# Kernel tuning notes

Measured on AMD Instinct MI355X. Metric: run time of the kernel, lower is better.

Reference implementation:

```python
import jax, jax.numpy as jnp
import numpy as np


def _lstm(x_seq, Wih, Whh, bih, bhh, hidden):
    """Single-layer batch_first LSTM, PyTorch gate order (i,f,g,o).
    x_seq: [B, T, D_in]. Returns (outputs [B, T, H], h_T [B, H])."""
    B = x_seq.shape[0]
    h0 = jnp.zeros((B, hidden), x_seq.dtype)
    c0 = jnp.zeros((B, hidden), x_seq.dtype)

    def step(carry, x_t):
        h, c = carry
        gates = x_t @ Wih.T + bih + h @ Whh.T + bhh  # [B, 4H]
        i, f, g, o = jnp.split(gates, 4, axis=-1)
        i = jax.nn.sigmoid(i)
        f = jax.nn.sigmoid(f)
        g = jnp.tanh(g)
        o = jax.nn.sigmoid(o)
        c = f * c + i * g
        h = o * jnp.tanh(c)
        return (h, c), h

    (hT, _), hs = jax.lax.scan(step, (h0, c0), jnp.swapaxes(x_seq, 0, 1))
    return jnp.swapaxes(hs, 0, 1), hT


def setup_inputs() -> dict:
    key = jax.random.key(0)
    ks = jax.random.split(key, 20)
    B, T = 4096, 140
    W = 0.1  # weight scale to keep gates out of saturation
    inp = {"x": jax.random.normal(ks[0], (B, 1, T), jnp.float32)}
    shapes = {
        "Wih_e1": (512, 1), "Whh_e1": (512, 128), "bih_e1": (512,), "bhh_e1": (512,),
        "Wih_e2": (256, 128), "Whh_e2": (256, 64), "bih_e2": (256,), "bhh_e2": (256,),
        "Wih_d1": (512, 64), "Whh_d1": (512, 128), "bih_d1": (512,), "bhh_d1": (512,),
        "Wih_d2": (4, 128), "Whh_d2": (4, 1), "bih_d2": (4,), "bhh_d2": (4,),
    }
    for i, (name, shp) in enumerate(shapes.items()):
        inp[name] = jax.random.normal(ks[i + 1], shp, jnp.float32) * W
    return inp


def reference(x, Wih_e1, Whh_e1, bih_e1, bhh_e1,
              Wih_e2, Whh_e2, bih_e2, bhh_e2,
              Wih_d1, Whh_d1, bih_d1, bhh_d1,
              Wih_d2, Whh_d2, bih_d2, bhh_d2):
    T = 140
    # x: [B,1,140] -> [B,140,1]
    x_enc = x[:, 0, :, None]
    _, h1 = _lstm(x_enc, Wih_e1, Whh_e1, bih_e1, bhh_e1, 128)  # h1: [B,128]
    # faithful to original bug: hn1 [1,B,128] fed as batch_first input (batch=1, seq=B)
    hn1_seq = h1[None, :, :]
    _, z = _lstm(hn1_seq, Wih_e2, Whh_e2, bih_e2, bhh_e2, 64)  # z: [1,64]
    dec_in = jnp.broadcast_to(z[:, None, :], (1, T, 64))
    out1, _ = _lstm(dec_in, Wih_d1, Whh_d1, bih_d1, bhh_d1, 128)  # [1,140,128]
    out2, _ = _lstm(out1, Wih_d2, Whh_d2, bih_d2, bhh_d2, 1)      # [1,140,1]
    recon = out2[..., 0][:, None, :]  # [1,1,140]
    return recon
```

## Files before the change

kernel.cpp:

```cpp
#include <hip/hip_runtime.h>
#include <hip/hip_bf16.h>


__device__ __forceinline__ float sigm(float x) {
  return 1.0f / (1.0f + __expf(-x));
}
__device__ __forceinline__ float tanh_fast(float x) {
  return 1.0f - 2.0f / (__expf(2.0f * x) + 1.0f);
}

__device__ __forceinline__ void wg_barrier() {
  asm volatile("s_waitcnt lgkmcnt(0)\n\ts_barrier" ::: "memory");
}

template <int CTRL>
__device__ __forceinline__ float dppmv(float v) {
  return __int_as_float(__builtin_amdgcn_update_dpp(
      0, __float_as_int(v), CTRL, 0xF, 0xF, true));
}
#define DPP_XOR1   0xB1
#define DPP_XOR2   0x4E
#define DPP_ROT1   0x93
#define DPP_HMIRR  0x141
#define DPP_MIRR   0x140

__device__ __forceinline__ int swzc(int k) { return k + ((k >> 5) << 2); }

#define A_BB 16

__global__ __launch_bounds__(512, 2) void lstm_e1_kernel(
    const float* __restrict__ x,
    const float* __restrict__ Wih,
    const float* __restrict__ Whh,
    const float* __restrict__ bih,
    const float* __restrict__ bhh,
    float* __restrict__ h1_out)
{
  const int j    = threadIdx.x;
  const int lane = j & 63;
  const int w    = j >> 6;
  const int u    = w * 16 + (lane >> 2);
  const int q    = lane & 3;
  const int b0   = blockIdx.x * A_BB;

  __shared__ float Hs[2][A_BB][144];
  __shared__ float xs[2][A_BB];

  for (int i = j; i < A_BB * 144; i += 512) ((float*)Hs[0])[i] = 0.0f;
  if (j < A_BB) xs[0][j] = x[(b0 + j) * 140];

  float wr[4][32];
#pragma unroll
  for (int g = 0; g < 4; ++g)
#pragma unroll
    for (int k = 0; k < 32; k += 4)
      *(float4*)&wr[g][k] = *(const float4*)&Whh[(g * 128 + u) * 128 + q * 32 + k];

  float wih[4], bs[4];
#pragma unroll
  for (int g = 0; g < 4; ++g) {
    wih[g] = Wih[g * 128 + u];
    bs[g]  = bih[g * 128 + u] + bhh[g * 128 + u];
  }

  float c[4]  = {0.f, 0.f, 0.f, 0.f};
  float hr[4] = {0.f, 0.f, 0.f, 0.f};
  __syncthreads();

  int cur = 0;
  for (int t = 0; t < 140; ++t) {
    const int nxt = cur ^ 1;

    float R[4][4];
#pragma unroll
    for (int g = 0; g < 4; ++g)
#pragma unroll
      for (int i = 0; i < 4; ++i) R[g][i] = 0.0f;

#pragma unroll
    for (int s = 0; s < 4; ++s) {
      if (s) {
#pragma unroll
        for (int g = 0; g < 4; ++g)
#pragma unroll
          for (int i = 0; i < 4; ++i) R[g][i] = dppmv<DPP_ROT1>(R[g][i]);
      }
      const int cch = (q - 1 - s) & 3;
      const float* hbase = &Hs[cur][cch * 4][q * 36];
#pragma unroll
      for (int i = 0; i < 4; ++i) {
        const float* hrow = hbase + i * 144;
#pragma unroll
        for (int kk = 0; kk < 8; ++kk) {
          const float4 hv = *(const float4*)&hrow[kk * 4];
#pragma unroll
          for (int g = 0; g < 4; ++g) {
            R[g][i] = __builtin_fmaf(wr[g][kk * 4 + 0], hv.x, R[g][i]);
            R[g][i] = __builtin_fmaf(wr[g][kk * 4 + 1], hv.y, R[g][i]);
            R[g][i] = __builtin_fmaf(wr[g][kk * 4 + 2], hv.z, R[g][i]);
            R[g][i] = __builtin_fmaf(wr[g][kk * 4 + 3], hv.w, R[g][i]);
          }
        }
      }
    }

    if (j < A_BB && (t + 1) < 140) xs[nxt][j] = x[(b0 + j) * 140 + t + 1];

    const float4 xv = *(const float4*)&xs[cur][q * 4];
    const float xa[4] = {xv.x, xv.y, xv.z, xv.w};
#pragma unroll
    for (int i = 0; i < 4; ++i) {
      const float gi = sigm(R[0][i] + __builtin_fmaf(wih[0], xa[i], bs[0]));
      const float gf = sigm(R[1][i] + __builtin_fmaf(wih[1], xa[i], bs[1]));
      const float gg = tanh_fast(R[2][i] + __builtin_fmaf(wih[2], xa[i], bs[2]));
      const float go = sigm(R[3][i] + __builtin_fmaf(wih[3], xa[i], bs[3]));
      c[i]  = gf * c[i] + gi * gg;
      hr[i] = go * tanh_fast(c[i]);
      Hs[nxt][q * 4 + i][swzc(u)] = hr[i];
    }
    wg_barrier();
    cur = nxt;
  }

#pragma unroll
  for (int i = 0; i < 4; ++i)
    h1_out[(b0 + q * 4 + i) * 128 + u] = hr[i];
}

__global__ __launch_bounds__(256, 1) void u_pre_kernel(
    const float* __restrict__ h1,
    const float* __restrict__ Wih,
    const float* __restrict__ bih,
    const float* __restrict__ bhh,
    float* __restrict__ Up)
{
  const int t = blockIdx.x;
  const int j = threadIdx.x;
  __shared__ float hs[128];
  if (j < 128) hs[j] = h1[t * 128 + j];
  __syncthreads();
  float acc = bih[j] + bhh[j];
#pragma unroll
  for (int k = 0; k < 128; k += 4) {
    const float4 hv = *(const float4*)&hs[k];
    const float4 wv = *(const float4*)&Wih[j * 128 + k];
    acc += wv.x * hv.x + wv.y * hv.y + wv.z * hv.z + wv.w * hv.w;
  }
  Up[t * 256 + (j & 63) * 4 + (j >> 6)] = acc;
}

__global__ __launch_bounds__(512, 1) void lstm_e2_scan_kernel(
    const float4* __restrict__ Up,
    const float* __restrict__ Whh,
    float* __restrict__ z_out)
{
  const int j = threadIdx.x;
  const int u = j >> 3;
  const int o = j & 7;

  __shared__ float hb[2][64];

  float wr[4][8];
#pragma unroll
  for (int g = 0; g < 4; ++g) {
    *(float4*)&wr[g][0] = *(const float4*)&Whh[(g * 64 + u) * 64 + o * 8];
    *(float4*)&wr[g][4] = *(const float4*)&Whh[(g * 64 + u) * 64 + o * 8 + 4];
  }

  if (j < 64) hb[0][j] = 0.0f;
  float c = 0.0f, h = 0.0f;

  float4 U0 = Up[u];
  float4 U1 = Up[64 + u];
  __syncthreads();

  int cur = 0;
#pragma unroll 1
  for (int t = 0; t < 4096; t += 2) {
#pragma unroll
    for (int half = 0; half < 2; ++half) {
      const int tp = (t + 2 + half < 4096) ? (t + 2 + half) : 4095;
      const float4 Unew = Up[tp * 64 + u];
      const float4 Ucur = half ? U1 : U0;

      const float4 hv0 = *(const float4*)&hb[cur][o * 8];
      const float4 hv1 = *(const float4*)&hb[cur][o * 8 + 4];
      float a0, a1, a2, a3;
      a0 = wr[0][0] * hv0.x; a1 = wr[1][0] * hv0.x; a2 = wr[2][0] * hv0.x; a3 = wr[3][0] * hv0.x;
      a0 = __builtin_fmaf(wr[0][1], hv0.y, a0); a1 = __builtin_fmaf(wr[1][1], hv0.y, a1);
      a2 = __builtin_fmaf(wr[2][1], hv0.y, a2); a3 = __builtin_fmaf(wr[3][1], hv0.y, a3);
      a0 = __builtin_fmaf(wr[0][2], hv0.z, a0); a1 = __builtin_fmaf(wr[1][2], hv0.z, a1);
      a2 = __builtin_fmaf(wr[2][2], hv0.z, a2); a3 = __builtin_fmaf(wr[3][2], hv0.z, a3);
      a0 = __builtin_fmaf(wr[0][3], hv0.w, a0); a1 = __builtin_fmaf(wr[1][3], hv0.w, a1);
      a2 = __builtin_fmaf(wr[2][3], hv0.w, a2); a3 = __builtin_fmaf(wr[3][3], hv0.w, a3);
      a0 = __builtin_fmaf(wr[0][4], hv1.x, a0); a1 = __builtin_fmaf(wr[1][4], hv1.x, a1);
      a2 = __builtin_fmaf(wr[2][4], hv1.x, a2); a3 = __builtin_fmaf(wr[3][4], hv1.x, a3);
      a0 = __builtin_fmaf(wr[0][5], hv1.y, a0); a1 = __builtin_fmaf(wr[1][5], hv1.y, a1);
      a2 = __builtin_fmaf(wr[2][5], hv1.y, a2); a3 = __builtin_fmaf(wr[3][5], hv1.y, a3);
      a0 = __builtin_fmaf(wr[0][6], hv1.z, a0); a1 = __builtin_fmaf(wr[1][6], hv1.z, a1);
      a2 = __builtin_fmaf(wr[2][6], hv1.z, a2); a3 = __builtin_fmaf(wr[3][6], hv1.z, a3);
      a0 = __builtin_fmaf(wr[0][7], hv1.w, a0); a1 = __builtin_fmaf(wr[1][7], hv1.w, a1);
      a2 = __builtin_fmaf(wr[2][7], hv1.w, a2); a3 = __builtin_fmaf(wr[3][7], hv1.w, a3);

      a0 += dppmv<DPP_XOR1>(a0);  a1 += dppmv<DPP_XOR1>(a1);
      a2 += dppmv<DPP_XOR1>(a2);  a3 += dppmv<DPP_XOR1>(a3);
      a0 += dppmv<DPP_XOR2>(a0);  a1 += dppmv<DPP_XOR2>(a1);
      a2 += dppmv<DPP_XOR2>(a2);  a3 += dppmv<DPP_XOR2>(a3);
      a0 += dppmv<DPP_HMIRR>(a0); a1 += dppmv<DPP_HMIRR>(a1);
      a2 += dppmv<DPP_HMIRR>(a2); a3 += dppmv<DPP_HMIRR>(a3);

      const float gi = sigm(a0 + Ucur.x);
      const float gf = sigm(a1 + Ucur.y);
      const float gg = tanh_fast(a2 + Ucur.z);
      const float go = sigm(a3 + Ucur.w);
      c = gf * c + gi * gg;
      h = go * tanh_fast(c);
      if (o == 0) hb[cur ^ 1][u] = h;
      if (half) U1 = Unew; else U0 = Unew;
      wg_barrier();
      cur ^= 1;
    }
  }
  if (o == 0) z_out[u] = h;
}

__global__ __launch_bounds__(512, 1) void lstm_dec_kernel(
    const float* __restrict__ z,
    const float* __restrict__ Wih1,
    const float* __restrict__ Whh1,
    const float* __restrict__ bih1,
    const float* __restrict__ bhh1,
    const float* __restrict__ Wih2,
    const float* __restrict__ Whh2,
    const float* __restrict__ bih2,
    const float* __restrict__ bhh2,
    float* __restrict__ out)
{
  const int j = threadIdx.x;
  const int u = j >> 2;
  const int q = j & 3;

  __shared__ float hb[2][144];
  __shared__ float zs[64];
  __shared__ float act4[4];

  if (j < 64) zs[j] = z[j];
  if (j < 144) hb[0][j] = 0.0f;
  __syncthreads();

  float wr[4][32];
#pragma unroll
  for (int g = 0; g < 4; ++g)
#pragma unroll
    for (int k = 0; k < 32; k += 4)
      *(float4*)&wr[g][k] = *(const float4*)&Whh1[(g * 128 + u) * 128 + q * 32 + k];

  float pre0[4];
#pragma unroll
  for (int g = 0; g < 4; ++g) {
    float acc = bih1[g * 128 + u] + bhh1[g * 128 + u];
#pragma unroll
    for (int k = 0; k < 64; k += 4) {
      const float4 zv = *(const float4*)&zs[k];
      const float4 wv = *(const float4*)&Wih1[(g * 128 + u) * 64 + k];
      acc += wv.x * zv.x + wv.y * zv.y + wv.z * zv.z + wv.w * zv.w;
    }
    pre0[g] = acc;
  }

  const int g2  = j >> 4;
  const int i16 = j & 15;
  float w2d[8] = {0,0,0,0,0,0,0,0};
  if (j < 64) {
#pragma unroll
    for (int e = 0; e < 8; ++e) w2d[e] = Wih2[g2 * 128 + i16 * 8 + e];
  }
  const float bb2_0 = bih2[0] + bhh2[0], wh2_0 = Whh2[0];
  const float bb2_1 = bih2[1] + bhh2[1], wh2_1 = Whh2[1];
  const float bb2_2 = bih2[2] + bhh2[2], wh2_2 = Whh2[2];
  const float bb2_3 = bih2[3] + bhh2[3], wh2_3 = Whh2[3];

  float c1 = 0.0f;
  float c2 = 0.0f, h2 = 0.0f;

  int cur = 0;
  for (int t = 0; t < 140; ++t) {
    float a0 = 0.f, a1 = 0.f, a2 = 0.f, a3 = 0.f;
#pragma unroll
    for (int kk = 0; kk < 8; ++kk) {
      const float4 hv = *(const float4*)&hb[cur][q * 36 + kk * 4];
      a0 = __builtin_fmaf(wr[0][kk*4+0], hv.x, a0); a0 = __builtin_fmaf(wr[0][kk*4+1], hv.y, a0);
      a0 = __builtin_fmaf(wr[0][kk*4+2], hv.z, a0); a0 = __builtin_fmaf(wr[0][kk*4+3], hv.w, a0);
      a1 = __builtin_fmaf(wr[1][kk*4+0], hv.x, a1); a1 = __builtin_fmaf(wr[1][kk*4+1], hv.y, a1);
      a1 = __builtin_fmaf(wr[1][kk*4+2], hv.z, a1); a1 = __builtin_fmaf(wr[1][kk*4+3], hv.w, a1);
      a2 = __builtin_fmaf(wr[2][kk*4+0], hv.x, a2); a2 = __builtin_fmaf(wr[2][kk*4+1], hv.y, a2);
      a2 = __builtin_fmaf(wr[2][kk*4+2], hv.z, a2); a2 = __builtin_fmaf(wr[2][kk*4+3], hv.w, a2);
      a3 = __builtin_fmaf(wr[3][kk*4+0], hv.x, a3); a3 = __builtin_fmaf(wr[3][kk*4+1], hv.y, a3);
      a3 = __builtin_fmaf(wr[3][kk*4+2], hv.z, a3); a3 = __builtin_fmaf(wr[3][kk*4+3], hv.w, a3);
    }
    a0 += dppmv<DPP_XOR1>(a0); a0 += dppmv<DPP_XOR2>(a0);
    a1 += dppmv<DPP_XOR1>(a1); a1 += dppmv<DPP_XOR2>(a1);
    a2 += dppmv<DPP_XOR1>(a2); a2 += dppmv<DPP_XOR2>(a2);
    a3 += dppmv<DPP_XOR1>(a3); a3 += dppmv<DPP_XOR2>(a3);

    const float gi = sigm(a0 + pre0[0]);
    const float gf = sigm(a1 + pre0[1]);
    const float gg = tanh_fast(a2 + pre0[2]);
    const float go = sigm(a3 + pre0[3]);
    c1 = gf * c1 + gi * gg;
    const float h1v = go * tanh_fast(c1);
    if (q == 0) hb[cur ^ 1][swzc(u)] = h1v;
    wg_barrier();
    cur ^= 1;

    if (j < 64) {
      const int kb = i16 * 8;
      const float4 hA = *(const float4*)&hb[cur][swzc(kb)];
      const float4 hB = *(const float4*)&hb[cur][swzc(kb) + 4];
      float p = hA.x * w2d[0];
      p = __builtin_fmaf(hA.y, w2d[1], p);
      p = __builtin_fmaf(hA.z, w2d[2], p);
      p = __builtin_fmaf(hA.w, w2d[3], p);
      p = __builtin_fmaf(hB.x, w2d[4], p);
      p = __builtin_fmaf(hB.y, w2d[5], p);
      p = __builtin_fmaf(hB.z, w2d[6], p);
      p = __builtin_fmaf(hB.w, w2d[7], p);
      p += dppmv<DPP_XOR1>(p);
      p += dppmv<DPP_XOR2>(p);
      p += dppmv<DPP_HMIRR>(p);
      p += dppmv<DPP_MIRR>(p);
      if (i16 == 0) act4[g2] = p;
      const float4 acts = *(const float4*)&act4[0];
      const float gi2 = sigm(acts.x + bb2_0 + wh2_0 * h2);
      const float gf2 = sigm(acts.y + bb2_1 + wh2_1 * h2);
      const float gg2 = tanh_fast(acts.z + bb2_2 + wh2_2 * h2);
      const float go2 = sigm(acts.w + bb2_3 + wh2_3 * h2);
      c2 = gf2 * c2 + gi2 * gg2;
      h2 = go2 * tanh_fast(c2);
      if (j == 0) out[t] = h2;
    }
  }
}

extern "C" void kernel_launch(void* const* d_in, const int* in_sizes, int n_in,
                              void* d_out, int out_size, void* d_ws, size_t ws_size,
                              hipStream_t stream) {
  const float* x      = (const float*)d_in[0];
  const float* Wih_e1 = (const float*)d_in[1];
  const float* Whh_e1 = (const float*)d_in[2];
  const float* bih_e1 = (const float*)d_in[3];
  const float* bhh_e1 = (const float*)d_in[4];
  const float* Wih_e2 = (const float*)d_in[5];
  const float* Whh_e2 = (const float*)d_in[6];
  const float* bih_e2 = (const float*)d_in[7];
  const float* bhh_e2 = (const float*)d_in[8];
  const float* Wih_d1 = (const float*)d_in[9];
  const float* Whh_d1 = (const float*)d_in[10];
  const float* bih_d1 = (const float*)d_in[11];
  const float* bhh_d1 = (const float*)d_in[12];
  const float* Wih_d2 = (const float*)d_in[13];
  const float* Whh_d2 = (const float*)d_in[14];
  const float* bih_d2 = (const float*)d_in[15];
  const float* bhh_d2 = (const float*)d_in[16];

  float* out = (float*)d_out;

  float* h1 = (float*)d_ws;
  float* Up = h1 + 4096 * 128;
  float* zb = Up + 4096 * 256;

  lstm_e1_kernel<<<4096 / A_BB, 512, 0, stream>>>(x, Wih_e1, Whh_e1, bih_e1, bhh_e1, h1);
  u_pre_kernel<<<4096, 256, 0, stream>>>(h1, Wih_e2, bih_e2, bhh_e2, Up);
  lstm_e2_scan_kernel<<<1, 512, 0, stream>>>((const float4*)Up, Whh_e2, zb);
  lstm_dec_kernel<<<1, 512, 0, stream>>>(zb, Wih_d1, Whh_d1, bih_d1, bhh_d1,
                                         Wih_d2, Whh_d2, bih_d2, bhh_d2, out);
}
```

Baseline: 3.986 ms.

## Use packed FP32 FMA and single-wavefront e2 scan; double units per e1 thread

The encoder-2 scan moves from eight wavefronts with DPP reductions and workgroup barriers to one 64-thread wavefront. Each lane now computes a full 64-wide dot product with packed v_pk_fma_f32 and syncs only through an LDS wait, which targets barrier and reduction latency on the 4096-step serial chain. The e1 kernel halves its thread count, gives each thread two hidden units using packed FMAs, and issues the next x load earlier. The cost is much higher register pressure: e1 now holds 256 weight floats per thread, risking spills or low occupancy. Each e2 step is also a longer dependent FMA chain per lane.

```diff
diff --git a/kernel.cpp b/kernel.cpp
--- a/kernel.cpp
+++ b/kernel.cpp
@@ -2,6 +2,14 @@
 #include <hip/hip_bf16.h>
 
 
+typedef float v2f __attribute__((ext_vector_type(2)));
+
+__device__ __forceinline__ v2f pk_fma(v2f a, v2f b, v2f c) {
+  v2f d;
+  asm("v_pk_fma_f32 %0, %1, %2, %3" : "=v"(d) : "v"(a), "v"(b), "v"(c));
+  return d;
+}
+
 __device__ __forceinline__ float sigm(float x) {
   return 1.0f / (1.0f + __expf(-x));
 }
@@ -11,6 +19,9 @@
 
 __device__ __forceinline__ void wg_barrier() {
   asm volatile("s_waitcnt lgkmcnt(0)\n\ts_barrier" ::: "memory");
+}
+__device__ __forceinline__ void lds_fence() {
+  asm volatile("s_waitcnt lgkmcnt(0)" ::: "memory");
 }
 
 template <int CTRL>
@@ -28,7 +39,7 @@
 
 #define A_BB 16
 
-__global__ __launch_bounds__(512, 2) void lstm_e1_kernel(
+__global__ __launch_bounds__(256, 1) void lstm_e1_kernel(
     const float* __restrict__ x,
     const float* __restrict__ Wih,
     const float* __restrict__ Whh,
@@ -39,43 +50,60 @@
   const int j    = threadIdx.x;
   const int lane = j & 63;
   const int w    = j >> 6;
-  const int u    = w * 16 + (lane >> 2);
+  const int u16  = w * 16 + (lane >> 2);
   const int q    = lane & 3;
+  const int uA   = u16;
+  const int uB   = u16 + 64;
   const int b0   = blockIdx.x * A_BB;
 
   __shared__ float Hs[2][A_BB][144];
   __shared__ float xs[2][A_BB];
 
-  for (int i = j; i < A_BB * 144; i += 512) ((float*)Hs[0])[i] = 0.0f;
+  for (int i = j; i < A_BB * 144; i += 256) ((float*)Hs[0])[i] = 0.0f;
   if (j < A_BB) xs[0][j] = x[(b0 + j) * 140];
 
-  float wr[4][32];
+  v2f wA[4][16], wB[4][16];
 #pragma unroll
   for (int g = 0; g < 4; ++g)
 #pragma unroll
-    for (int k = 0; k < 32; k += 4)
-      *(float4*)&wr[g][k] = *(const float4*)&Whh[(g * 128 + u) * 128 + q * 32 + k];
-
-  float wih[4], bs[4];
+    for (int k = 0; k < 32; k += 4) {
+      const float4 a = *(const float4*)&Whh[(g * 128 + uA) * 128 + q * 32 + k];
+      wA[g][k / 2 + 0].x = a.x; wA[g][k / 2 + 0].y = a.y;
+      wA[g][k / 2 + 1].x = a.z; wA[g][k / 2 + 1].y = a.w;
+      const float4 b = *(const float4*)&Whh[(g * 128 + uB) * 128 + q * 32 + k];
+      wB[g][k / 2 + 0].x = b.x; wB[g][k / 2 + 0].y = b.y;
+      wB[g][k / 2 + 1].x = b.z; wB[g][k / 2 + 1].y = b.w;
+    }
+
+  float wihA[4], bsA[4], wihB[4], bsB[4];
 #pragma unroll
   for (int g = 0; g < 4; ++g) {
-    wih[g] = Wih[g * 128 + u];
-    bs[g]  = bih[g * 128 + u] + bhh[g * 128 + u];
-  }
-
-  float c[4]  = {0.f, 0.f, 0.f, 0.f};
-  float hr[4] = {0.f, 0.f, 0.f, 0.f};
+    wihA[g] = Wih[g * 128 + uA];
+    bsA[g]  = bih[g * 128 + uA] + bhh[g * 128 + uA];
+    wihB[g] = Wih[g * 128 + uB];
+    bsB[g]  = bih[g * 128 + uB] + bhh[g * 128 + uB];
+  }
+
+  float cA[4] = {0,0,0,0}, hA[4] = {0,0,0,0};
+  float cB[4] = {0,0,0,0}, hB[4] = {0,0,0,0};
   __syncthreads();
 
   int cur = 0;
   for (int t = 0; t < 140; ++t) {
     const int nxt = cur ^ 1;
 
-    float R[4][4];
+    float xnext = 0.0f;
+    const bool do_x = (j < A_BB) && (t + 1) < 140;
+    if (do_x) xnext = x[(b0 + j) * 140 + t + 1];
+
+    v2f RA[4][4], RB[4][4];
 #pragma unroll
     for (int g = 0; g < 4; ++g)
 #pragma unroll
-      for (int i = 0; i < 4; ++i) R[g][i] = 0.0f;
+      for (int i = 0; i < 4; ++i) {
+        RA[g][i].x = 0.f; RA[g][i].y = 0.f;
+        RB[g][i].x = 0.f; RB[g][i].y = 0.f;
+      }
 
 #pragma unroll
     for (int s = 0; s < 4; ++s) {
@@ -83,7 +111,12 @@
 #pragma unroll
         for (int g = 0; g < 4; ++g)
 #pragma unroll
-          for (int i = 0; i < 4; ++i) R[g][i] = dppmv<DPP_ROT1>(R[g][i]);
+          for (int i = 0; i < 4; ++i) {
+            RA[g][i].x = dppmv<DPP_ROT1>(RA[g][i].x);
+            RA[g][i].y = dppmv<DPP_ROT1>(RA[g][i].y);
+            RB[g][i].x = dppmv<DPP_ROT1>(RB[g][i].x);
+            RB[g][i].y = dppmv<DPP_ROT1>(RB[g][i].y);
+          }
       }
       const int cch = (q - 1 - s) & 3;
       const float* hbase = &Hs[cur][cch * 4][q * 36];
@@ -93,38 +126,53 @@
 #pragma unroll
         for (int kk = 0; kk < 8; ++kk) {
           const float4 hv = *(const float4*)&hrow[kk * 4];
+          v2f h01; h01.x = hv.x; h01.y = hv.y;
+          v2f h23; h23.x = hv.z; h23.y = hv.w;
 #pragma unroll
           for (int g = 0; g < 4; ++g) {
-            R[g][i] = __builtin_fmaf(wr[g][kk * 4 + 0], hv.x, R[g][i]);
-            R[g][i] = __builtin_fmaf(wr[g][kk * 4 + 1], hv.y, R[g][i]);
-            R[g][i] = __builtin_fmaf(wr[g][kk * 4 + 2], hv.z, R[g][i]);
-            R[g][i] = __builtin_fmaf(wr[g][kk * 4 + 3], hv.w, R[g][i]);
+            RA[g][i] = pk_fma(wA[g][2 * kk + 0], h01, RA[g][i]);
+            RA[g][i] = pk_fma(wA[g][2 * kk + 1], h23, RA[g][i]);
+            RB[g][i] = pk_fma(wB[g][2 * kk + 0], h01, RB[g][i]);
+            RB[g][i] = pk_fma(wB[g][2 * kk + 1], h23, RB[g][i]);
           }
         }
       }
     }
 
-    if (j < A_BB && (t + 1) < 140) xs[nxt][j] = x[(b0 + j) * 140 + t + 1];
+    if (do_x) xs[nxt][j] = xnext;
 
     const float4 xv = *(const float4*)&xs[cur][q * 4];
     const float xa[4] = {xv.x, xv.y, xv.z, xv.w};
 #pragma unroll
     for (int i = 0; i < 4; ++i) {
-      const float gi = sigm(R[0][i] + __builtin_fmaf(wih[0], xa[i], bs[0]));
-      const float gf = sigm(R[1][i] + __builtin_fmaf(wih[1], xa[i], bs[1]));
-      const float gg = tanh_fast(R[2][i] + __builtin_fmaf(wih[2], xa[i], bs[2]));
-      const float go = sigm(R[3][i] + __builtin_fmaf(wih[3], xa[i], bs[3]));
-      c[i]  = gf * c[i] + gi * gg;
-      hr[i] = go * tanh_fast(c[i]);
-      Hs[nxt][q * 4 + i][swzc(u)] = hr[i];
+      {
+        const float gi = sigm(RA[0][i].x + RA[0][i].y + __builtin_fmaf(wihA[0], xa[i], bsA[0]));
+        const float gf = sigm(RA[1][i].x + RA[1][i].y + __builtin_fmaf(wihA[1], xa[i], bsA[1]));
+        const float gg = tanh_fast(RA[2][i].x + RA[2][i].y + __builtin_fmaf(wihA[2], xa[i], bsA[2]));
+        const float go = sigm(RA[3][i].x + RA[3][i].y + __builtin_fmaf(wihA[3], xa[i], bsA[3]));
+        cA[i] = gf * cA[i] + gi * gg;
+        hA[i] = go * tanh_fast(cA[i]);
+        Hs[nxt][q * 4 + i][swzc(uA)] = hA[i];
+      }
+      {
+        const float gi = sigm(RB[0][i].x + RB[0][i].y + __builtin_fmaf(wihB[0], xa[i], bsB[0]));
+        const float gf = sigm(RB[1][i].x + RB[1][i].y + __builtin_fmaf(wihB[1], xa[i], bsB[1]));
+        const float gg = tanh_fast(RB[2][i].x + RB[2][i].y + __builtin_fmaf(wihB[2], xa[i], bsB[2]));
+        const float go = sigm(RB[3][i].x + RB[3][i].y + __builtin_fmaf(wihB[3], xa[i], bsB[3]));
+        cB[i] = gf * cB[i] + gi * gg;
+        hB[i] = go * tanh_fast(cB[i]);
+        Hs[nxt][q * 4 + i][swzc(uB)] = hB[i];
+      }
     }
     wg_barrier();
     cur = nxt;
   }
 
 #pragma unroll
-  for (int i = 0; i < 4; ++i)
-    h1_out[(b0 + q * 4 + i) * 128 + u] = hr[i];
+  for (int i = 0; i < 4; ++i) {
+    h1_out[(b0 + q * 4 + i) * 128 + uA] = hA[i];
+    h1_out[(b0 + q * 4 + i) * 128 + uB] = hB[i];
+  }
 }
 
 __global__ __launch_bounds__(256, 1) void u_pre_kernel(
@@ -149,79 +197,81 @@
   Up[t * 256 + (j & 63) * 4 + (j >> 6)] = acc;
 }
 
-__global__ __launch_bounds__(512, 1) void lstm_e2_scan_kernel(
+__global__ __launch_bounds__(64, 1) void lstm_e2_scan_kernel(
     const float4* __restrict__ Up,
     const float* __restrict__ Whh,
     float* __restrict__ z_out)
 {
-  const int j = threadIdx.x;
-  const int u = j >> 3;
-  const int o = j & 7;
-
-  __shared__ float hb[2][64];
-
-  float wr[4][8];
-#pragma unroll
-  for (int g = 0; g < 4; ++g) {
-    *(float4*)&wr[g][0] = *(const float4*)&Whh[(g * 64 + u) * 64 + o * 8];
-    *(float4*)&wr[g][4] = *(const float4*)&Whh[(g * 64 + u) * 64 + o * 8 + 4];
-  }
-
-  if (j < 64) hb[0][j] = 0.0f;
+  const int u = threadIdx.x;
+  __shared__ float hbuf[64];
+
+  v2f wr2[4][32];
+#pragma unroll
+  for (int g = 0; g < 4; ++g)
+#pragma unroll
+    for (int k = 0; k < 64; k += 4) {
+      const float4 t4 = *(const float4*)&Whh[(g * 64 + u) * 64 + k];
+      wr2[g][k / 2 + 0].x = t4.x; wr2[g][k / 2 + 0].y = t4.y;
+      wr2[g][k / 2 + 1].x = t4.z; wr2[g][k / 2 + 1].y = t4.w;
+    }
+
   float c = 0.0f, h = 0.0f;
-
-  float4 U0 = Up[u];
-  float4 U1 = Up[64 + u];
-  __syncthreads();
-
-  int cur = 0;
+  hbuf[u] = 0.0f;
+  lds_fence();
+
+  float4 U0 = Up[0 * 64 + u];
+  float4 U1 = Up[1 * 64 + u];
+  float4 U2 = Up[2 * 64 + u];
+  float4 U3 = Up[3 * 64 + u];
+
+  const float4* hb4 = (const float4*)hbuf;
+
+#define SCAN_STEP(UREG, TNEXT)                                                \
+  do {                                                                        \
+    v2f A0, A1, A2, A3;                                                       \
+    A0.x = 0.f; A0.y = 0.f; A1 = A0; A2 = A0; A3 = A0;                        \
+    _Pragma("unroll")                                                         \
+    for (int grp = 0; grp < 4; ++grp) {                                       \
+      float4 Hh[4];                                                           \
+      _Pragma("unroll")                                                       \
+      for (int r = 0; r < 4; ++r) Hh[r] = hb4[grp * 4 + r];                   \
+      _Pragma("unroll")                                                       \
+      for (int r = 0; r < 4; ++r) {                                           \
+        const int p = (grp * 4 + r) * 2;                                      \
+        v2f hx; hx.x = Hh[r].x; hx.y = Hh[r].y;                               \
+        v2f hy; hy.x = Hh[r].z; hy.y = Hh[r].w;                               \
+        A0 = pk_fma(wr2[0][p], hx, A0); A0 = pk_fma(wr2[0][p + 1], hy, A0);   \
+        A1 = pk_fma(wr2[1][p], hx, A1); A1 = pk_fma(wr2[1][p + 1], hy, A1);   \
+        A2 = pk_fma(wr2[2][p], hx, A2); A2 = pk_fma(wr2[2][p + 1], hy, A2);   \
+        A3 = pk_fma(wr2[3][p], hx, A3); A3 = pk_fma(wr2[3][p + 1], hy, A3);   \
+      }                                                                       \
+    }                                                                         \
+    const float a0 = A0.x + A0.y, a1 = A1.x + A1.y;                           \
+    const float a2 = A2.x + A2.y, a3 = A3.x + A3.y;                           \
+    const float gi = sigm(a0 + UREG.x);                                       \
+    const float gf = sigm(a1 + UREG.y);                                       \
+    const float gg = tanh_fast(a2 + UREG.z);                                  \
+    const float go = sigm(a3 + UREG.w);                                       \
+    c = gf * c + gi * gg;                                                     \
+    h = go * tanh_fast(c);                                                    \
+    hbuf[u] = h;                                                              \
+    {                                                                         \
+      const int tp_ = ((TNEXT) < 4096) ? (TNEXT) : 4095;                      \
+      UREG = Up[tp_ * 64 + u];                                                \
+    }                                                                         \
+    lds_fence();                                                              \
+  } while (0)
+
 #pragma unroll 1
-  for (int t = 0; t < 4096; t += 2) {
-#pragma unroll
-    for (int half = 0; half < 2; ++half) {
-      const int tp = (t + 2 + half < 4096) ? (t + 2 + half) : 4095;
-      const float4 Unew = Up[tp * 64 + u];
-      const float4 Ucur = half ? U1 : U0;
-
-      const float4 hv0 = *(const float4*)&hb[cur][o * 8];
-      const float4 hv1 = *(const float4*)&hb[cur][o * 8 + 4];
-      float a0, a1, a2, a3;
-      a0 = wr[0][0] * hv0.x; a1 = wr[1][0] * hv0.x; a2 = wr[2][0] * hv0.x; a3 = wr[3][0] * hv0.x;
-      a0 = __builtin_fmaf(wr[0][1], hv0.y, a0); a1 = __builtin_fmaf(wr[1][1], hv0.y, a1);
-      a2 = __builtin_fmaf(wr[2][1], hv0.y, a2); a3 = __builtin_fmaf(wr[3][1], hv0.y, a3);
-      a0 = __builtin_fmaf(wr[0][2], hv0.z, a0); a1 = __builtin_fmaf(wr[1][2], hv0.z, a1);
-      a2 = __builtin_fmaf(wr[2][2], hv0.z, a2); a3 = __builtin_fmaf(wr[3][2], hv0.z, a3);
-      a0 = __builtin_fmaf(wr[0][3], hv0.w, a0); a1 = __builtin_fmaf(wr[1][3], hv0.w, a1);
-      a2 = __builtin_fmaf(wr[2][3], hv0.w, a2); a3 = __builtin_fmaf(wr[3][3], hv0.w, a3);
-      a0 = __builtin_fmaf(wr[0][4], hv1.x, a0); a1 = __builtin_fmaf(wr[1][4], hv1.x, a1);
-      a2 = __builtin_fmaf(wr[2][4], hv1.x, a2); a3 = __builtin_fmaf(wr[3][4], hv1.x, a3);
-      a0 = __builtin_fmaf(wr[0][5], hv1.y, a0); a1 = __builtin_fmaf(wr[1][5], hv1.y, a1);
-      a2 = __builtin_fmaf(wr[2][5], hv1.y, a2); a3 = __builtin_fmaf(wr[3][5], hv1.y, a3);
-      a0 = __builtin_fmaf(wr[0][6], hv1.z, a0); a1 = __builtin_fmaf(wr[1][6], hv1.z, a1);
-      a2 = __builtin_fmaf(wr[2][6], hv1.z, a2); a3 = __builtin_fmaf(wr[3][6], hv1.z, a3);
-      a0 = __builtin_fmaf(wr[0][7], hv1.w, a0); a1 = __builtin_fmaf(wr[1][7], hv1.w, a1);
-      a2 = __builtin_fmaf(wr[2][7], hv1.w, a2); a3 = __builtin_fmaf(wr[3][7], hv1.w, a3);
-
-      a0 += dppmv<DPP_XOR1>(a0);  a1 += dppmv<DPP_XOR1>(a1);
-      a2 += dppmv<DPP_XOR1>(a2);  a3 += dppmv<DPP_XOR1>(a3);
-      a0 += dppmv<DPP_XOR2>(a0);  a1 += dppmv<DPP_XOR2>(a1);
-      a2 += dppmv<DPP_XOR2>(a2);  a3 += dppmv<DPP_XOR2>(a3);
-      a0 += dppmv<DPP_HMIRR>(a0); a1 += dppmv<DPP_HMIRR>(a1);
-      a2 += dppmv<DPP_HMIRR>(a2); a3 += dppmv<DPP_HMIRR>(a3);
-
-      const float gi = sigm(a0 + Ucur.x);
-      const float gf = sigm(a1 + Ucur.y);
-      const float gg = tanh_fast(a2 + Ucur.z);
-      const float go = sigm(a3 + Ucur.w);
-      c = gf * c + gi * gg;
-      h = go * tanh_fast(c);
-      if (o == 0) hb[cur ^ 1][u] = h;
-      if (half) U1 = Unew; else U0 = Unew;
-      wg_barrier();
-      cur ^= 1;
-    }
-  }
-  if (o == 0) z_out[u] = h;
+  for (int t = 0; t < 4096; t += 4) {
+    SCAN_STEP(U0, t + 4);
+    SCAN_STEP(U1, t + 5);
+    SCAN_STEP(U2, t + 6);
+    SCAN_STEP(U3, t + 7);
+  }
+#undef SCAN_STEP
+
+  z_out[u] = h;
 }
 
 __global__ __launch_bounds__(512, 1) void lstm_dec_kernel(
@@ -240,12 +290,12 @@
   const int u = j >> 2;
   const int q = j & 3;
 
-  __shared__ float hb[2][144];
+  __shared__ float hd[2][144];
   __shared__ float zs[64];
   __shared__ float act4[4];
 
   if (j < 64) zs[j] = z[j];
-  if (j < 144) hb[0][j] = 0.0f;
+  if (j < 144) hd[0][j] = 0.0f;
   __syncthreads();
 
   float wr[4][32];
@@ -288,7 +338,7 @@
     float a0 = 0.f, a1 = 0.f, a2 = 0.f, a3 = 0.f;
 #pragma unroll
     for (int kk = 0; kk < 8; ++kk) {
-      const float4 hv = *(const float4*)&hb[cur][q * 36 + kk * 4];
+      const float4 hv = *(const float4*)&hd[cur][q * 36 + kk * 4];
       a0 = __builtin_fmaf(wr[0][kk*4+0], hv.x, a0); a0 = __builtin_fmaf(wr[0][kk*4+1], hv.y, a0);
       a0 = __builtin_fmaf(wr[0][kk*4+2], hv.z, a0); a0 = __builtin_fmaf(wr[0][kk*4+3], hv.w, a0);
       a1 = __builtin_fmaf(wr[1][kk*4+0], hv.x, a1); a1 = __builtin_fmaf(wr[1][kk*4+1], hv.y, a1);
@@ -309,14 +359,14 @@
     const float go = sigm(a3 + pre0[3]);
     c1 = gf * c1 + gi * gg;
     const float h1v = go * tanh_fast(c1);
-    if (q == 0) hb[cur ^ 1][swzc(u)] = h1v;
+    if (q == 0) hd[cur ^ 1][swzc(u)] = h1v;
     wg_barrier();
     cur ^= 1;
 
     if (j < 64) {
       const int kb = i16 * 8;
-      const float4 hA = *(const float4*)&hb[cur][swzc(kb)];
-      const float4 hB = *(const float4*)&hb[cur][swzc(kb) + 4];
+      const float4 hA = *(const float4*)&hd[cur][swzc(kb)];
+      const float4 hB = *(const float4*)&hd[cur][swzc(kb) + 4];
       float p = hA.x * w2d[0];
       p = __builtin_fmaf(hA.y, w2d[1], p);
       p = __builtin_fmaf(hA.z, w2d[2], p);
@@ -369,9 +419,9 @@
   float* Up = h1 + 4096 * 128;
   float* zb = Up + 4096 * 256;
 
-  lstm_e1_kernel<<<4096 / A_BB, 512, 0, stream>>>(x, Wih_e1, Whh_e1, bih_e1, bhh_e1, h1);
+  lstm_e1_kernel<<<4096 / A_BB, 256, 0, stream>>>(x, Wih_e1, Whh_e1, bih_e1, bhh_e1, h1);
   u_pre_kernel<<<4096, 256, 0, stream>>>(h1, Wih_e2, bih_e2, bhh_e2, Up);
-  lstm_e2_scan_kernel<<<1, 512, 0, stream>>>((const float4*)Up, Whh_e2, zb);
+  lstm_e2_scan_kernel<<<1, 64, 0, stream>>>((const float4*)Up, Whh_e2, zb);
   lstm_dec_kernel<<<1, 512, 0, stream>>>(zb, Wih_d1, Whh_d1, bih_d1, bhh_d1,
                                          Wih_d2, Whh_d2, bih_d2, bhh_d2, out);
 }
```

After: 8.326 ms. 2.09x slower.

## Use packed FP32 FMA in encoder kernels and shrink e2 scan to two waves

Applied to the files above, without the earlier changes.

The e1 recurrent matvec now uses v_pk_fma_f32 on paired weights and hidden values, which halves the FMA instruction count and adds one add per gate at the end. The serial e2 scan (4096 steps) moves from 512 threads with 8 lanes per unit to 128 threads with 2 lanes per unit. Each thread does 32-wide packed dot products, and the cross-lane reduction drops to a single DPP step. The aim is to cut per-step latency on the serial chain through fewer waves at the barrier and fewer shuffles, at the cost of more serial FMA work per thread.

```diff
diff --git a/kernel.cpp b/kernel.cpp
--- a/kernel.cpp
+++ b/kernel.cpp
@@ -1,6 +1,14 @@
 #include <hip/hip_runtime.h>
 #include <hip/hip_bf16.h>
 
+
+typedef float v2f __attribute__((ext_vector_type(2)));
+
+__device__ __forceinline__ v2f pk_fma(v2f a, v2f b, v2f c) {
+  v2f d;
+  asm("v_pk_fma_f32 %0, %1, %2, %3" : "=v"(d) : "v"(a), "v"(b), "v"(c));
+  return d;
+}
 
 __device__ __forceinline__ float sigm(float x) {
   return 1.0f / (1.0f + __expf(-x));
@@ -49,12 +57,15 @@
   for (int i = j; i < A_BB * 144; i += 512) ((float*)Hs[0])[i] = 0.0f;
   if (j < A_BB) xs[0][j] = x[(b0 + j) * 140];
 
-  float wr[4][32];
+  v2f wr2[4][16];
 #pragma unroll
   for (int g = 0; g < 4; ++g)
 #pragma unroll
-    for (int k = 0; k < 32; k += 4)
-      *(float4*)&wr[g][k] = *(const float4*)&Whh[(g * 128 + u) * 128 + q * 32 + k];
+    for (int k = 0; k < 32; k += 4) {
+      const float4 t4 = *(const float4*)&Whh[(g * 128 + u) * 128 + q * 32 + k];
+      wr2[g][k / 2 + 0].x = t4.x; wr2[g][k / 2 + 0].y = t4.y;
+      wr2[g][k / 2 + 1].x = t4.z; wr2[g][k / 2 + 1].y = t4.w;
+    }
 
   float wih[4], bs[4];
 #pragma unroll
@@ -71,11 +82,11 @@
   for (int t = 0; t < 140; ++t) {
     const int nxt = cur ^ 1;
 
-    float R[4][4];
+    v2f R2[4][4];
 #pragma unroll
     for (int g = 0; g < 4; ++g)
 #pragma unroll
-      for (int i = 0; i < 4; ++i) R[g][i] = 0.0f;
+      for (int i = 0; i < 4; ++i) { R2[g][i].x = 0.f; R2[g][i].y = 0.f; }
 
 #pragma unroll
     for (int s = 0; s < 4; ++s) {
@@ -83,7 +94,10 @@
 #pragma unroll
         for (int g = 0; g < 4; ++g)
 #pragma unroll
-          for (int i = 0; i < 4; ++i) R[g][i] = dppmv<DPP_ROT1>(R[g][i]);
+          for (int i = 0; i < 4; ++i) {
+            R2[g][i].x = dppmv<DPP_ROT1>(R2[g][i].x);
+            R2[g][i].y = dppmv<DPP_ROT1>(R2[g][i].y);
+          }
       }
       const int cch = (q - 1 - s) & 3;
       const float* hbase = &Hs[cur][cch * 4][q * 36];
@@ -93,12 +107,12 @@
 #pragma unroll
         for (int kk = 0; kk < 8; ++kk) {
           const float4 hv = *(const float4*)&hrow[kk * 4];
+          v2f h01; h01.x = hv.x; h01.y = hv.y;
+          v2f h23; h23.x = hv.z; h23.y = hv.w;
 #pragma unroll
           for (int g = 0; g < 4; ++g) {
-            R[g][i] = __builtin_fmaf(wr[g][kk * 4 + 0], hv.x, R[g][i]);
-            R[g][i] = __builtin_fmaf(wr[g][kk * 4 + 1], hv.y, R[g][i]);
-            R[g][i] = __builtin_fmaf(wr[g][kk * 4 + 2], hv.z, R[g][i]);
-            R[g][i] = __builtin_fmaf(wr[g][kk * 4 + 3], hv.w, R[g][i]);
+            R2[g][i] = pk_fma(wr2[g][2 * kk + 0], h01, R2[g][i]);
+            R2[g][i] = pk_fma(wr2[g][2 * kk + 1], h23, R2[g][i]);
           }
         }
       }
@@ -110,10 +124,10 @@
     const float xa[4] = {xv.x, xv.y, xv.z, xv.w};
 #pragma unroll
     for (int i = 0; i < 4; ++i) {
-      const float gi = sigm(R[0][i] + __builtin_fmaf(wih[0], xa[i], bs[0]));
-      const float gf = sigm(R[1][i] + __builtin_fmaf(wih[1], xa[i], bs[1]));
-      const float gg = tanh_fast(R[2][i] + __builtin_fmaf(wih[2], xa[i], bs[2]));
-      const float go = sigm(R[3][i] + __builtin_fmaf(wih[3], xa[i], bs[3]));
+      const float gi = sigm(R2[0][i].x + R2[0][i].y + __builtin_fmaf(wih[0], xa[i], bs[0]));
+      const float gf = sigm(R2[1][i].x + R2[1][i].y + __builtin_fmaf(wih[1], xa[i], bs[1]));
+      const float gg = tanh_fast(R2[2][i].x + R2[2][i].y + __builtin_fmaf(wih[2], xa[i], bs[2]));
+      const float go = sigm(R2[3][i].x + R2[3][i].y + __builtin_fmaf(wih[3], xa[i], bs[3]));
       c[i]  = gf * c[i] + gi * gg;
       hr[i] = go * tanh_fast(c[i]);
       Hs[nxt][q * 4 + i][swzc(u)] = hr[i];
@@ -149,29 +163,32 @@
   Up[t * 256 + (j & 63) * 4 + (j >> 6)] = acc;
 }
 
-__global__ __launch_bounds__(512, 1) void lstm_e2_scan_kernel(
+__global__ __launch_bounds__(128, 1) void lstm_e2_scan_kernel(
     const float4* __restrict__ Up,
     const float* __restrict__ Whh,
     float* __restrict__ z_out)
 {
   const int j = threadIdx.x;
-  const int u = j >> 3;
-  const int o = j & 7;
+  const int u = j >> 1;
+  const int p = j & 1;
 
   __shared__ float hb[2][64];
 
-  float wr[4][8];
-#pragma unroll
-  for (int g = 0; g < 4; ++g) {
-    *(float4*)&wr[g][0] = *(const float4*)&Whh[(g * 64 + u) * 64 + o * 8];
-    *(float4*)&wr[g][4] = *(const float4*)&Whh[(g * 64 + u) * 64 + o * 8 + 4];
-  }
+  v2f wr2[4][16];
+#pragma unroll
+  for (int g = 0; g < 4; ++g)
+#pragma unroll
+    for (int k = 0; k < 32; k += 4) {
+      const float4 t4 = *(const float4*)&Whh[(g * 64 + u) * 64 + p * 32 + k];
+      wr2[g][k / 2 + 0].x = t4.x; wr2[g][k / 2 + 0].y = t4.y;
+      wr2[g][k / 2 + 1].x = t4.z; wr2[g][k / 2 + 1].y = t4.w;
+    }
 
   if (j < 64) hb[0][j] = 0.0f;
   float c = 0.0f, h = 0.0f;
 
-  float4 U0 = Up[u];
-  float4 U1 = Up[64 + u];
+  float4 U0 = Up[0 * 64 + u];
+  float4 U1 = Up[1 * 64 + u];
   __syncthreads();
 
   int cur = 0;
@@ -183,31 +200,25 @@
       const float4 Unew = Up[tp * 64 + u];
       const float4 Ucur = half ? U1 : U0;
 
-      const float4 hv0 = *(const float4*)&hb[cur][o * 8];
-      const float4 hv1 = *(const float4*)&hb[cur][o * 8 + 4];
-      float a0, a1, a2, a3;
-      a0 = wr[0][0] * hv0.x; a1 = wr[1][0] * hv0.x; a2 = wr[2][0] * hv0.x; a3 = wr[3][0] * hv0.x;
-      a0 = __builtin_fmaf(wr[0][1], hv0.y, a0); a1 = __builtin_fmaf(wr[1][1], hv0.y, a1);
-      a2 = __builtin_fmaf(wr[2][1], hv0.y, a2); a3 = __builtin_fmaf(wr[3][1], hv0.y, a3);
-      a0 = __builtin_fmaf(wr[0][2], hv0.z, a0); a1 = __builtin_fmaf(wr[1][2], hv0.z, a1);
-      a2 = __builtin_fmaf(wr[2][2], hv0.z, a2); a3 = __builtin_fmaf(wr[3][2], hv0.z, a3);
-      a0 = __builtin_fmaf(wr[0][3], hv0.w, a0); a1 = __builtin_fmaf(wr[1][3], hv0.w, a1);
-      a2 = __builtin_fmaf(wr[2][3], hv0.w, a2); a3 = __builtin_fmaf(wr[3][3], hv0.w, a3);
-      a0 = __builtin_fmaf(wr[0][4], hv1.x, a0); a1 = __builtin_fmaf(wr[1][4], hv1.x, a1);
-      a2 = __builtin_fmaf(wr[2][4], hv1.x, a2); a3 = __builtin_fmaf(wr[3][4], hv1.x, a3);
-      a0 = __builtin_fmaf(wr[0][5], hv1.y, a0); a1 = __builtin_fmaf(wr[1][5], hv1.y, a1);
-      a2 = __builtin_fmaf(wr[2][5], hv1.y, a2); a3 = __builtin_fmaf(wr[3][5], hv1.y, a3);
-      a0 = __builtin_fmaf(wr[0][6], hv1.z, a0); a1 = __builtin_fmaf(wr[1][6], hv1.z, a1);
-      a2 = __builtin_fmaf(wr[2][6], hv1.z, a2); a3 = __builtin_fmaf(wr[3][6], hv1.z, a3);
-      a0 = __builtin_fmaf(wr[0][7], hv1.w, a0); a1 = __builtin_fmaf(wr[1][7], hv1.w, a1);
-      a2 = __builtin_fmaf(wr[2][7], hv1.w, a2); a3 = __builtin_fmaf(wr[3][7], hv1.w, a3);
-
-      a0 += dppmv<DPP_XOR1>(a0);  a1 += dppmv<DPP_XOR1>(a1);
-      a2 += dppmv<DPP_XOR1>(a2);  a3 += dppmv<DPP_XOR1>(a3);
-      a0 += dppmv<DPP_XOR2>(a0);  a1 += dppmv<DPP_XOR2>(a1);
-      a2 += dppmv<DPP_XOR2>(a2);  a3 += dppmv<DPP_XOR2>(a3);
-      a0 += dppmv<DPP_HMIRR>(a0); a1 += dppmv<DPP_HMIRR>(a1);
-      a2 += dppmv<DPP_HMIRR>(a2); a3 += dppmv<DPP_HMIRR>(a3);
+      const float* hrow = &hb[cur][p * 32];
+      v2f A0, A1, A2, A3;
+      A0.x = 0.f; A0.y = 0.f; A1 = A0; A2 = A0; A3 = A0;
+#pragma unroll
+      for (int kk = 0; kk < 8; ++kk) {
+        const float4 hv = *(const float4*)&hrow[kk * 4];
+        v2f hx; hx.x = hv.x; hx.y = hv.y;
+        v2f hy; hy.x = hv.z; hy.y = hv.w;
+        A0 = pk_fma(wr2[0][2 * kk], hx, A0); A0 = pk_fma(wr2[0][2 * kk + 1], hy, A0);
+        A1 = pk_fma(wr2[1][2 * kk], hx, A1); A1 = pk_fma(wr2[1][2 * kk + 1], hy, A1);
+        A2 = pk_fma(wr2[2][2 * kk], hx, A2); A2 = pk_fma(wr2[2][2 * kk + 1], hy, A2);
+        A3 = pk_fma(wr2[3][2 * kk], hx, A3); A3 = pk_fma(wr2[3][2 * kk + 1], hy, A3);
+      }
+      float a0 = A0.x + A0.y, a1 = A1.x + A1.y;
+      float a2 = A2.x + A2.y, a3 = A3.x + A3.y;
+      a0 += dppmv<DPP_XOR1>(a0);
+      a1 += dppmv<DPP_XOR1>(a1);
+      a2 += dppmv<DPP_XOR1>(a2);
+      a3 += dppmv<DPP_XOR1>(a3);
 
       const float gi = sigm(a0 + Ucur.x);
       const float gf = sigm(a1 + Ucur.y);
@@ -215,13 +226,13 @@
       const float go = sigm(a3 + Ucur.w);
       c = gf * c + gi * gg;
       h = go * tanh_fast(c);
-      if (o == 0) hb[cur ^ 1][u] = h;
+      if (p == 0) hb[cur ^ 1][u] = h;
       if (half) U1 = Unew; else U0 = Unew;
       wg_barrier();
       cur ^= 1;
     }
   }
-  if (o == 0) z_out[u] = h;
+  if (p == 0) z_out[u] = h;
 }
 
 __global__ __launch_bounds__(512, 1) void lstm_dec_kernel(
@@ -240,12 +251,12 @@
   const int u = j >> 2;
   const int q = j & 3;
 
-  __shared__ float hb[2][144];
+  __shared__ float hd[2][144];
   __shared__ float zs[64];
   __shared__ float act4[4];
 
   if (j < 64) zs[j] = z[j];
-  if (j < 144) hb[0][j] = 0.0f;
+  if (j < 144) hd[0][j] = 0.0f;
   __syncthreads();
 
   float wr[4][32];
@@ -288,7 +299,7 @@
     float a0 = 0.f, a1 = 0.f, a2 = 0.f, a3 = 0.f;
 #pragma unroll
     for (int kk = 0; kk < 8; ++kk) {
-      const float4 hv = *(const float4*)&hb[cur][q * 36 + kk * 4];
+      const float4 hv = *(const float4*)&hd[cur][q * 36 + kk * 4];
       a0 = __builtin_fmaf(wr[0][kk*4+0], hv.x, a0); a0 = __builtin_fmaf(wr[0][kk*4+1], hv.y, a0);
       a0 = __builtin_fmaf(wr[0][kk*4+2], hv.z, a0); a0 = __builtin_fmaf(wr[0][kk*4+3], hv.w, a0);
       a1 = __builtin_fmaf(wr[1][kk*4+0], hv.x, a1); a1 = __builtin_fmaf(wr[1][kk*4+1], hv.y, a1);
@@ -309,14 +320,14 @@
     const float go = sigm(a3 + pre0[3]);
     c1 = gf * c1 + gi * gg;
     const float h1v = go * tanh_fast(c1);
-    if (q == 0) hb[cur ^ 1][swzc(u)] = h1v;
+    if (q == 0) hd[cur ^ 1][swzc(u)] = h1v;
     wg_barrier();
     cur ^= 1;
 
     if (j < 64) {
       const int kb = i16 * 8;
-      const float4 hA = *(const float4*)&hb[cur][swzc(kb)];
-      const float4 hB = *(const float4*)&hb[cur][swzc(kb) + 4];
+      const float4 hA = *(const float4*)&hd[cur][swzc(kb)];
+      const float4 hB = *(const float4*)&hd[cur][swzc(kb) + 4];
       float p = hA.x * w2d[0];
       p = __builtin_fmaf(hA.y, w2d[1], p);
       p = __builtin_fmaf(hA.z, w2d[2], p);
@@ -371,7 +382,7 @@
 
   lstm_e1_kernel<<<4096 / A_BB, 512, 0, stream>>>(x, Wih_e1, Whh_e1, bih_e1, bhh_e1, h1);
   u_pre_kernel<<<4096, 256, 0, stream>>>(h1, Wih_e2, bih_e2, bhh_e2, Up);
-  lstm_e2_scan_kernel<<<1, 512, 0, stream>>>((const float4*)Up, Whh_e2, zb);
+  lstm_e2_scan_kernel<<<1, 128, 0, stream>>>((const float4*)Up, Whh_e2, zb);
   lstm_dec_kernel<<<1, 512, 0, stream>>>(zb, Wih_d1, Whh_d1, bih_d1, bhh_d1,
                                          Wih_d2, Whh_d2, bih_d2, bhh_d2, out);
 }
```

Measured after the change: 3.424 ms. 1.16x faster.
